# Performance work log

Hardware: AMD Instinct MI355X
Metric: run time of the kernel (lower is better)

The kernel has to match this reference:

```python
import jax, jax.numpy as jnp
import numpy as np

SIGMA1 = 1.0        # RBF bandwidth for kernel1
DYADIC_ORDER = 1    # dyadic grid refinement
LAMBD = 1.0         # ridge regularizer
INPUT_SCALE = 0.1   # keep signature-kernel values in fp32 range


def rbf_gram(X, Y, sigma):
    # X: (N,S,D), Y: (M,T,D) -> (N,M,S,T), sigkernel RBFKernel: exp(-||x-y||^2 / sigma)
    x2 = jnp.sum(X * X, axis=-1)  # (N,S)
    y2 = jnp.sum(Y * Y, axis=-1)  # (M,T)
    xy = jnp.einsum('nsd,mtd->nmst', X, Y)
    d2 = x2[:, None, :, None] + y2[None, :, None, :] - 2.0 * xy
    return jnp.exp(-d2 / sigma)


def linear_gram(X, Y):
    # sigkernel LinearKernel: inner product Gram
    return jnp.einsum('nsd,mtd->nmst', X, Y)


def sig_kernel_gram(G, dyadic_order):
    """Solve the Goursat PDE for the signature kernel on a dyadic grid.

    G: (N,M,S,T) static-kernel Gram. Returns (N,M) signature-kernel Gram.
    Update (sigkernel explicit scheme):
      k[i+1,j+1] = (k[i+1,j] + k[i,j+1]) * (1 + inc/2 + inc^2/12)
                   - k[i,j] * (1 - inc^2/12)
    """
    N, M, S, T = G.shape
    # double increments of the static kernel
    inc = G[:, :, 1:, 1:] - G[:, :, 1:, :-1] - G[:, :, :-1, 1:] + G[:, :, :-1, :-1]
    f = 2 ** dyadic_order
    inc = jnp.repeat(jnp.repeat(inc, f, axis=2), f, axis=3) / float(f * f)
    B = N * M
    P, Q = (S - 1) * f, (T - 1) * f
    inc = inc.reshape(B, P, Q)
    C1 = 1.0 + 0.5 * inc + inc * inc * (1.0 / 12.0)
    C2 = 1.0 - inc * inc * (1.0 / 12.0)
    ones_b = jnp.ones((B,), G.dtype)

    def row_step(prev_row, coeffs):
        c1, c2 = coeffs  # (B,Q) each

        def col_step(left, v):
            c1j, c2j, pj, pjm1 = v  # each (B,)
            new = (left + pj) * c1j - pjm1 * c2j
            return new, new

        xs = (c1.T, c2.T, prev_row[:, 1:].T, prev_row[:, :-1].T)  # (Q,B)
        _, vals = jax.lax.scan(col_step, ones_b, xs)  # (Q,B)
        new_row = jnp.concatenate([ones_b[:, None], vals.T], axis=1)  # (B,Q+1)
        return new_row, None

    row0 = jnp.ones((B, Q + 1), G.dtype)
    last_row, _ = jax.lax.scan(row_step, row0, (jnp.moveaxis(C1, 1, 0), jnp.moveaxis(C2, 1, 0)))
    return last_row[:, -1].reshape(N, M)


def cmmd(x, y, z):
    N = x.shape[0]
    K = sig_kernel_gram(rbf_gram(x, x, SIGMA1), DYADIC_ORDER)
    L_gen = sig_kernel_gram(linear_gram(y, y), DYADIC_ORDER)
    L_true = sig_kernel_gram(linear_gram(z, z), DYADIC_ORDER)
    L_mix = sig_kernel_gram(linear_gram(y, z), DYADIC_ORDER)
    Ktildeinv = jnp.linalg.inv(K + jnp.eye(N, dtype=K.dtype) * LAMBD)
    A = K @ Ktildeinv  # shared left factor

    def tr(L):
        return jnp.trace(A @ (L @ Ktildeinv))

    return tr(L_gen) + tr(L_true) - 2.0 * tr(L_mix)


def setup_inputs() -> dict:
    key = jax.random.key(0)
    k1, k2, k3 = jax.random.split(key, 3)
    shape = (64, 33, 8)
    return {
        'x': jax.random.normal(k1, shape, dtype=jnp.float32) * INPUT_SCALE,
        'y': jax.random.normal(k2, shape, dtype=jnp.float32) * INPUT_SCALE,
        'z': jax.random.normal(k3, shape, dtype=jnp.float32) * INPUT_SCALE,
    }


def reference(x, y, z):
    return cmmd(x, y, z)
```

## Files before the change

### kernel.cpp

```cpp
#include <hip/hip_runtime.h>
#include <hip/hip_fp16.h>
#include <math.h>


#define SLEN 33

__device__ __forceinline__ float rl(float v, int lane) {
    return __int_as_float(__builtin_amdgcn_readlane(__float_as_int(v), lane));
}

__device__ __forceinline__ void pde_item(int g, int loc,
                                         const float* __restrict__ x,
                                         const float* __restrict__ y,
                                         const float* __restrict__ z,
                                         float* __restrict__ ws,
                                         float4 (*Xi4)[66],
                                         __half (*incH)[1024]) {
    const int lane = threadIdx.x & 63;
    const int h = lane >> 5;
    const int p = lane & 31;

    int pair = 2 * loc + h, gi, gj;
    if (g == 3) {
        gi = pair >> 6; gj = pair & 63;
    } else {
        float ff = sqrtf(8.0f * (float)pair + 1.0f);
        gi = (int)((ff - 1.0f) * 0.5f);
        while ((gi + 1) * (gi + 2) / 2 <= pair) ++gi;
        while (gi * (gi + 1) / 2 > pair) --gi;
        gj = pair - gi * (gi + 1) / 2;
    }

    const float* Ap = (g == 0) ? x : ((g == 2) ? z : y);
    const float* Bp = (g == 0) ? x : ((g == 1) ? y : z);
    const float4* As = (const float4*)(Ap + gi * (SLEN * 8));
    const float4* Bs = (const float4*)(Bp + gj * (SLEN * 8));

    for (int k = p; k < 66; k += 32) Xi4[h][k] = As[k];
    float4 b0 = Bs[2*p],   b1 = Bs[2*p+1];
    float4 b2 = Bs[2*p+2], b3 = Bs[2*p+3];
    __syncthreads();

    if (g == 0) {
        float nprev;
        {
            float4 a0 = Xi4[h][0], a1 = Xi4[h][1];
            float d0=a0.x-b0.x,d1=a0.y-b0.y,d2=a0.z-b0.z,d3=a0.w-b0.w;
            float d4=a1.x-b1.x,d5=a1.y-b1.y,d6=a1.z-b1.z,d7=a1.w-b1.w;
            float da = d0*d0+d1*d1+d2*d2+d3*d3+d4*d4+d5*d5+d6*d6+d7*d7;
            float e0=a0.x-b2.x,e1=a0.y-b2.y,e2=a0.z-b2.z,e3=a0.w-b2.w;
            float e4=a1.x-b3.x,e5=a1.y-b3.y,e6=a1.z-b3.z,e7=a1.w-b3.w;
            float db = e0*e0+e1*e1+e2*e2+e3*e3+e4*e4+e5*e5+e6*e6+e7*e7;
            nprev = __expf(-db) - __expf(-da);
        }
        for (int k = 1; k <= 32; ++k) {
            float4 a0 = Xi4[h][2*k], a1 = Xi4[h][2*k+1];
            float d0=a0.x-b0.x,d1=a0.y-b0.y,d2=a0.z-b0.z,d3=a0.w-b0.w;
            float d4=a1.x-b1.x,d5=a1.y-b1.y,d6=a1.z-b1.z,d7=a1.w-b1.w;
            float da = d0*d0+d1*d1+d2*d2+d3*d3+d4*d4+d5*d5+d6*d6+d7*d7;
            float e0=a0.x-b2.x,e1=a0.y-b2.y,e2=a0.z-b2.z,e3=a0.w-b2.w;
            float e4=a1.x-b3.x,e5=a1.y-b3.y,e6=a1.z-b3.z,e7=a1.w-b3.w;
            float db = e0*e0+e1*e1+e2*e2+e3*e3+e4*e4+e5*e5+e6*e6+e7*e7;
            float diffk = __expf(-db) - __expf(-da);
            incH[h][(k-1)*32 + p] = __float2half(0.25f * (diffk - nprev));
            nprev = diffk;
        }
    } else {
        float e0=b2.x-b0.x, e1=b2.y-b0.y, e2=b2.z-b0.z, e3=b2.w-b0.w;
        float e4=b3.x-b1.x, e5=b3.y-b1.y, e6=b3.z-b1.z, e7=b3.w-b1.w;
        float4 a0 = Xi4[h][0], a1 = Xi4[h][1];
        #pragma unroll 4
        for (int k = 0; k < 32; ++k) {
            float4 a2 = Xi4[h][2*k+2], a3 = Xi4[h][2*k+3];
            float acc = (a2.x-a0.x)*e0 + (a2.y-a0.y)*e1
                      + (a2.z-a0.z)*e2 + (a2.w-a0.w)*e3
                      + (a3.x-a1.x)*e4 + (a3.y-a1.y)*e5
                      + (a3.z-a1.z)*e6 + (a3.w-a1.w)*e7;
            incH[h][k*32 + p] = __float2half(0.25f * acc);
            a0 = a2; a1 = a3;
        }
    }
    __syncthreads();

    float c01 = 1.0f, c10 = 1.0f, c11 = 1.0f, dcarry = 1.0f;
    const bool isrow0 = (p == 0);
    const __half* incrow = &incH[h][p * 32];
    #pragma unroll 4
    for (int m = 0; m < 63; ++m) {
        float nb10 = __shfl_up(c10, 1);
        float nb11 = __shfl_up(c11, 1);
        int t = m - p;
        float incv = __half2float(incrow[t & 31]);
        float n0 = isrow0 ? 1.0f : nb10;
        float n1 = isrow0 ? 1.0f : nb11;
        bool t0 = (t == 0);
        float w0 = t0 ? 1.0f : c01;
        float w1 = t0 ? 1.0f : c11;
        float d  = t0 ? 1.0f : dcarry;
        float i2 = incv * incv * (1.0f / 12.0f);
        float C1 = 1.0f + 0.5f * incv + i2;
        float C2 = 1.0f - i2;
        float v00 = (w0  + n0 ) * C1 - d   * C2;
        float v01 = (v00 + n1 ) * C1 - n0  * C2;
        float v10 = (v00 + w1 ) * C1 - w0  * C2;
        float v11 = (v10 + v01) * C1 - v00 * C2;
        c01 = v01; c10 = v10; c11 = v11;
        dcarry = n1;
    }

    if (p == 31) {
        float* dst = ws + g * 4096;
        dst[gi * 64 + gj] = c11;
        if (g != 3) dst[gj * 64 + gi] = c11;
    }
}

__global__ __launch_bounds__(64, 5)
void pdeK_kernel(const float* __restrict__ x, const float* __restrict__ y,
                 const float* __restrict__ z, float* __restrict__ ws) {
    __shared__ float4 XiS[2][66];
    __shared__ __half incS[2][1024];
    pde_item(0, blockIdx.x, x, y, z, ws, XiS, incS);
}

__global__ __launch_bounds__(512, 4)
void pdeL_gj_trace_kernel(const float* __restrict__ x,
                          const float* __restrict__ y,
                          const float* __restrict__ z,
                          float* __restrict__ ws,
                          unsigned int* __restrict__ counter,
                          float* __restrict__ out) {
    union U {
        struct { float4 XiS[16][66]; __half incS[16][1024]; } pde;
        float Kls[64 * 65];
    };
    __shared__ U sm;
    __shared__ float prow[2][2][64];
    __shared__ float red[8];

    const int b   = blockIdx.x;
    const int tid = threadIdx.x;
    const int wv  = tid >> 6;

    if (b == 0) {
        const int c = tid & 63, w = wv;
        const float* K = ws;
        float m[8];
        #pragma unroll
        for (int i = 0; i < 8; ++i) {
            int r = w * 8 + i;
            m[i] = K[r * 64 + c] + ((r == c) ? 1.0f : 0.0f);
        }
        #pragma unroll 1
        for (int it = 0; it < 8; ++it) {
            #pragma unroll
            for (int j = 0; j < 4; ++j) {
                const int p0 = 8 * it + 2 * j, p1 = p0 + 1;
                const int i0 = 2 * j, i1 = i0 + 1;
                const int buf = j & 1;
                if (w == it) {
                    float x0 = m[i0], x1 = m[i1];
                    float a  = rl(x0, p0), bq = rl(x0, p1);
                    float cq = rl(x1, p0), dq = rl(x1, p1);
                    float dinv = 1.0f / (a * dq - bq * cq);
                    float P00 =  dq * dinv, P01 = -bq * dinv;
                    float P10 = -cq * dinv, P11 =  a  * dinv;
                    float sp0 = P00 * x0 + P01 * x1;
                    float sp1 = P10 * x0 + P11 * x1;
                    sp0 = (c == p0) ? P00 : ((c == p1) ? P01 : sp0);
                    sp1 = (c == p0) ? P10 : ((c == p1) ? P11 : sp1);
                    m[i0] = sp0; m[i1] = sp1;
                    prow[buf][0][c] = sp0;
                    prow[buf][1][c] = sp1;
                }
                __syncthreads();
                float s0  = prow[buf][0][c],  s1  = prow[buf][1][c];
                float q00 = prow[buf][0][p0], q01 = prow[buf][0][p1];
                float q10 = prow[buf][1][p0], q11 = prow[buf][1][p1];
                #pragma unroll
                for (int i = 0; i < 8; ++i) {
                    bool pivotRow = (w == it) && (i == i0 || i == i1);
                    float f0 = rl(m[i], p0);
                    float f1 = rl(m[i], p1);
                    float nv = m[i] - f0 * s0 - f1 * s1;
                    float wb0 = -(f0 * q00 + f1 * q10);
                    float wb1 = -(f0 * q01 + f1 * q11);
                    nv = (c == p0) ? wb0 : ((c == p1) ? wb1 : nv);
                    if (!pivotRow) m[i] = nv;
                }
            }
        }
        #pragma unroll
        for (int i = 0; i < 8; ++i)
            sm.Kls[(w * 8 + i) * 65 + c] = m[i];

        if (tid == 0) {
            while (atomicAdd(counter, 0u) < 516u)
                __builtin_amdgcn_s_sleep(2);
        }
        __syncthreads();
        __threadfence();

        const float* Lg = ws + 4096;
        const float* Lt = ws + 8192;
        const float* Lm = ws + 12288;
        float acc[8] = {0,0,0,0,0,0,0,0};
        #pragma unroll 2
        for (int k = 0; k < 64; ++k) {
            float rv = sm.Kls[k * 65 + c];
            #pragma unroll
            for (int i = 0; i < 8; ++i)
                acc[i] = fmaf(rl(m[i], k), rv, acc[i]);
        }
        float local = 0.0f;
        #pragma unroll
        for (int i = 0; i < 8; ++i) {
            int r = w * 8 + i;
            float lc = Lg[r * 64 + c] + Lt[r * 64 + c] - 2.0f * Lm[r * 64 + c];
            local += (m[i] - acc[i]) * lc;
        }
        #pragma unroll
        for (int off = 32; off > 0; off >>= 1)
            local += __shfl_down(local, off);
        if (c == 0) red[w] = local;
        __syncthreads();
        if (tid == 0) {
            float v = 0.0f;
            #pragma unroll
            for (int i = 0; i < 8; ++i) v += red[i];
            out[0] = v;
        }
    } else {
        int item = (b - 1) * 8 + wv;
        int g, loc;
        if (item < 1040)      { g = 1; loc = item; }
        else if (item < 2080) { g = 2; loc = item - 1040; }
        else                  { g = 3; loc = item - 2080; }
        pde_item(g, loc, x, y, z, ws, &sm.pde.XiS[2 * wv], &sm.pde.incS[2 * wv]);
        __syncthreads();
        if (tid == 0) {
            __threadfence();
            atomicAdd(counter, 1u);
        }
    }
}

extern "C" void kernel_launch(void* const* d_in, const int* in_sizes, int n_in,
                              void* d_out, int out_size, void* d_ws, size_t ws_size,
                              hipStream_t stream) {
    const float* x = (const float*)d_in[0];
    const float* y = (const float*)d_in[1];
    const float* z = (const float*)d_in[2];
    float* out = (float*)d_out;
    float* ws  = (float*)d_ws;
    unsigned int* counter = (unsigned int*)(ws + 16384);

    hipMemsetAsync(counter, 0, sizeof(unsigned int), stream);
    pdeK_kernel<<<1040, 64, 0, stream>>>(x, y, z, ws);
    pdeL_gj_trace_kernel<<<517, 512, 0, stream>>>(x, y, z, ws, counter, out);
}
```

Before: 103.3 us.

## Merge K-gram PDE kernel into single persistent kernel with counter-based sync

Folds the separate K-gram PDE launch into the main kernel as 130 extra 512-thread blocks, and adds a second completion counter. The Gauss-Jordan block now spin-waits on the K counter before inverting, then on the L counter before the trace. This removes one kernel launch and its boundary, and lets the K and L PDE work run concurrently. It relies on the K blocks being scheduled before the waiting block to avoid a stall, and it changes how the K work is packed onto CUs.

```diff
diff --git a/kernel.cpp b/kernel.cpp
--- a/kernel.cpp
+++ b/kernel.cpp
@@ -115,21 +115,13 @@
     }
 }
 
-__global__ __launch_bounds__(64, 5)
-void pdeK_kernel(const float* __restrict__ x, const float* __restrict__ y,
-                 const float* __restrict__ z, float* __restrict__ ws) {
-    __shared__ float4 XiS[2][66];
-    __shared__ __half incS[2][1024];
-    pde_item(0, blockIdx.x, x, y, z, ws, XiS, incS);
-}
-
 __global__ __launch_bounds__(512, 4)
-void pdeL_gj_trace_kernel(const float* __restrict__ x,
-                          const float* __restrict__ y,
-                          const float* __restrict__ z,
-                          float* __restrict__ ws,
-                          unsigned int* __restrict__ counter,
-                          float* __restrict__ out) {
+void mono_kernel(const float* __restrict__ x,
+                 const float* __restrict__ y,
+                 const float* __restrict__ z,
+                 float* __restrict__ ws,
+                 unsigned int* __restrict__ cnt,
+                 float* __restrict__ out) {
     union U {
         struct { float4 XiS[16][66]; __half incS[16][1024]; } pde;
         float Kls[64 * 65];
@@ -142,8 +134,37 @@
     const int tid = threadIdx.x;
     const int wv  = tid >> 6;
 
-    if (b == 0) {
+    if (b < 130) {
+        pde_item(0, b * 8 + wv, x, y, z, ws,
+                 &sm.pde.XiS[2 * wv], &sm.pde.incS[2 * wv]);
+        __syncthreads();
+        if (tid == 0) {
+            __threadfence();
+            atomicAdd(&cnt[0], 1u);
+        }
+    } else if (b > 130) {
+        int item = (b - 131) * 8 + wv;
+        int g, loc;
+        if (item < 1040)      { g = 1; loc = item; }
+        else if (item < 2080) { g = 2; loc = item - 1040; }
+        else                  { g = 3; loc = item - 2080; }
+        pde_item(g, loc, x, y, z, ws,
+                 &sm.pde.XiS[2 * wv], &sm.pde.incS[2 * wv]);
+        __syncthreads();
+        if (tid == 0) {
+            __threadfence();
+            atomicAdd(&cnt[1], 1u);
+        }
+    } else {
         const int c = tid & 63, w = wv;
+
+        if (tid == 0) {
+            while (atomicAdd(&cnt[0], 0u) < 130u)
+                __builtin_amdgcn_s_sleep(2);
+        }
+        __syncthreads();
+        __threadfence();
+
         const float* K = ws;
         float m[8];
         #pragma unroll
@@ -195,7 +216,7 @@
             sm.Kls[(w * 8 + i) * 65 + c] = m[i];
 
         if (tid == 0) {
-            while (atomicAdd(counter, 0u) < 516u)
+            while (atomicAdd(&cnt[1], 0u) < 516u)
                 __builtin_amdgcn_s_sleep(2);
         }
         __syncthreads();
@@ -230,18 +251,6 @@
             for (int i = 0; i < 8; ++i) v += red[i];
             out[0] = v;
         }
-    } else {
-        int item = (b - 1) * 8 + wv;
-        int g, loc;
-        if (item < 1040)      { g = 1; loc = item; }
-        else if (item < 2080) { g = 2; loc = item - 1040; }
-        else                  { g = 3; loc = item - 2080; }
-        pde_item(g, loc, x, y, z, ws, &sm.pde.XiS[2 * wv], &sm.pde.incS[2 * wv]);
-        __syncthreads();
-        if (tid == 0) {
-            __threadfence();
-            atomicAdd(counter, 1u);
-        }
     }
 }
 
@@ -253,9 +262,8 @@
     const float* z = (const float*)d_in[2];
     float* out = (float*)d_out;
     float* ws  = (float*)d_ws;
-    unsigned int* counter = (unsigned int*)(ws + 16384);
-
-    hipMemsetAsync(counter, 0, sizeof(unsigned int), stream);
-    pdeK_kernel<<<1040, 64, 0, stream>>>(x, y, z, ws);
-    pdeL_gj_trace_kernel<<<517, 512, 0, stream>>>(x, y, z, ws, counter, out);
-}
+    unsigned int* cnt = (unsigned int*)(ws + 16384);
+
+    hipMemsetAsync(cnt, 0, 2 * sizeof(unsigned int), stream);
+    mono_kernel<<<647, 512, 0, stream>>>(x, y, z, ws, cnt, out);
+}
```

Result: slower. 111.1 us (+7.6%).
